# Performance work log

Measured on AMD Instinct MI355X. Metric: run time of the kernel, lower is better.

## Reference

```python
import jax, jax.numpy as jnp
import numpy as np

DIM = 768
HID = 24576          # hidden_features (SAE dictionary size)
DENSE = 3072         # dense_hidden_features (MLP width)
NUM_LAYERS = 12
L = NUM_LAYERS * 2   # forward requires x.shape[1] == num_layers*2 (broadcast with decoder_b2)
B = 64
K = 16               # num_active_features


def setup_inputs() -> dict:
    key = jax.random.key(0)
    ks = jax.random.split(key, 10)
    s1 = 1.0 / np.sqrt(DIM)
    s2 = 1.0 / np.sqrt(DENSE)
    s3 = 1.0 / np.sqrt(HID)
    return {
        "x": jax.random.normal(ks[0], (B, L, DIM), dtype=jnp.float32),
        "encoder_w1": jax.random.uniform(ks[1], (DENSE, DIM), jnp.float32, -s1, s1),
        "encoder_b1": jnp.zeros((DENSE,), jnp.float32),
        "encoder_w2": jax.random.uniform(ks[2], (HID, DENSE), jnp.float32, -s2, s2),
        "encoder_b2": jnp.zeros((HID,), jnp.float32),
        "decoder_w1": jax.random.uniform(ks[3], (DENSE, HID), jnp.float32, -s3, s3),
        "decoder_b1": jnp.zeros((DENSE,), jnp.float32),
        "decoder_w2": jax.random.uniform(ks[4], (DIM, DENSE), jnp.float32, -s2, s2),
        "decoder_b2": jax.random.uniform(ks[5], (1, L, DIM), jnp.float32, -s1, s1),
    }


def reference(x, encoder_w1, encoder_b1, encoder_w2, encoder_b2,
              decoder_w1, decoder_b1, decoder_w2, decoder_b2):
    # subtract per-(layer,dim) decoder bias, dense encode, GELU (exact, matches nn.GELU)
    h = jax.nn.gelu(jnp.einsum('blc,dc->bld', x - decoder_b2, encoder_w1) + encoder_b1,
                    approximate=False)                         # [B, L, DENSE]
    z = jnp.einsum('bld,nd->bln', h, encoder_w2) + encoder_b2  # [B, L, HID]
    # topk mask: keep only K largest per (b, l), zero the rest (scatter of ones)
    _, idx = jax.lax.top_k(z, K)                               # [B, L, K]
    b_idx = jnp.arange(z.shape[0])[:, None, None]
    l_idx = jnp.arange(z.shape[1])[None, :, None]
    mask = jnp.zeros_like(z).at[b_idx, l_idx, idx].set(1.0)
    z = jax.nn.relu(z * mask)                                  # act_fn = ReLU
    # dense decode (full GEMM over mostly-zero hidden dim, as in the original)
    d = jax.nn.gelu(jnp.einsum('bln,dn->bld', z, decoder_w1) + decoder_b1,
                    approximate=False)                         # [B, L, DENSE]
    return jnp.einsum('bld,cd->blc', d, decoder_w2) + decoder_b2  # [B, L, DIM]
```

## Files before the change

### kernel.cpp

```cpp
#include <hip/hip_runtime.h>
#include <hip/hip_fp16.h>

#define DIM 768
#define HID 24576
#define DENSE 3072
#define LL 24
#define MROWS 1536
#define KSEL 16
#define NC 24
#define CAP 40
#define MF_TOT 96
#define ENC2_NT 96
#define DELTA 2e-3f

typedef _Float16 f16;
typedef __attribute__((ext_vector_type(8))) _Float16 f16x8;
typedef __attribute__((ext_vector_type(4))) float f32x4;
typedef const __attribute__((address_space(1))) char* gcp;
typedef __attribute__((address_space(3))) char* lcp;

__device__ __forceinline__ float gelu_exact(float x) {
    return 0.5f * x * (1.0f + erff(x * 0.7071067811865476f));
}

__device__ __forceinline__ void split8(const float4& v0, const float4& v1,
                                       f16x8& hi, f16x8& lo) {
    float vv[8] = {v0.x, v0.y, v0.z, v0.w, v1.x, v1.y, v1.z, v1.w};
#pragma unroll
    for (int j = 0; j < 8; ++j) {
        f16 h = (f16)vv[j];
        hi[j] = h;
        lo[j] = (f16)((vv[j] - (float)h) * 2048.0f);
    }
}


template <int KTOT, int RFTOT>
__global__ __launch_bounds__(256) void apack_kernel(
    const float* __restrict__ src, f16* __restrict__ dst) {
    int c = blockIdx.x * 4 + (threadIdx.x >> 6);
    int lane = threadIdx.x & 63;
    int rf = c % RFTOT, ks = c / RFTOT;
    int m = rf * 16 + (lane & 15);
    int k = ks * 32 + (lane >> 4) * 8;
    const float4* s = (const float4*)(src + (size_t)m * (KTOT * 32) + k);
    f16x8 hi, lo;
    split8(s[0], s[1], hi, lo);
    char* base = (char*)dst + (size_t)c * 2048 + lane * 16;
    *(f16x8*)base = hi;
    *(f16x8*)(base + 1024) = lo;
}

__global__ __launch_bounds__(256) void prep1_kernel(
    const float* __restrict__ x, const float* __restrict__ b2,
    f16* __restrict__ xcpk,
    const float* __restrict__ w1src, f16* __restrict__ W1pk) {
    int lane = threadIdx.x & 63;
    if (blockIdx.x < 576) {
        int c = blockIdx.x * 4 + (threadIdx.x >> 6);
        int rf = c % MF_TOT, ks = c / MF_TOT;
        int m = rf * 16 + (lane & 15);
        int k = ks * 32 + (lane >> 4) * 8;
        const float4* sx = (const float4*)(x + (size_t)m * DIM + k);
        const float4* sb = (const float4*)(b2 + (m % LL) * DIM + k);
        float4 v0 = sx[0], v1 = sx[1], b0 = sb[0], b1 = sb[1];
        v0.x -= b0.x; v0.y -= b0.y; v0.z -= b0.z; v0.w -= b0.w;
        v1.x -= b1.x; v1.y -= b1.y; v1.z -= b1.z; v1.w -= b1.w;
        f16x8 hi, lo;
        split8(v0, v1, hi, lo);
        char* base = (char*)xcpk + (size_t)c * 2048 + lane * 16;
        *(f16x8*)base = hi;
        *(f16x8*)(base + 1024) = lo;
    } else {
        int c = (blockIdx.x - 576) * 4 + (threadIdx.x >> 6);
        int nf = c & 7; int t = c >> 3; int ks = t % 24; int nb = t / 24;
        int n = nb * 128 + nf * 16 + (lane & 15);
        int k = ks * 32 + (lane >> 4) * 8;
        const float4* s = (const float4*)(w1src + (size_t)n * DIM + k);
        f16x8 hi, lo;
        split8(s[0], s[1], hi, lo);
        char* base = (char*)W1pk + (size_t)c * 2048 + lane * 16;
        *(f16x8*)base = hi;
        *(f16x8*)(base + 1024) = lo;
    }
}

template <int KTOT>
__global__ __launch_bounds__(256) void wpack_kernel(
    const float* __restrict__ src, f16* __restrict__ dst, int row0) {
    int c = blockIdx.x * 4 + (threadIdx.x >> 6);
    int lane = threadIdx.x & 63;
    int nf = c & 7; int t = c >> 3; int ks = t % KTOT; int nb = t / KTOT;
    int n = row0 + nb * 128 + nf * 16 + (lane & 15);
    int k = ks * 32 + (lane >> 4) * 8;
    const float4* s = (const float4*)(src + (size_t)n * (KTOT * 32) + k);
    f16x8 hi, lo;
    split8(s[0], s[1], hi, lo);
    char* base = (char*)dst + (size_t)c * 2048 + lane * 16;
    *(f16x8*)base = hi;
    *(f16x8*)(base + 1024) = lo;
}

__global__ __launch_bounds__(256) void prep2_kernel(
    const float* __restrict__ h, f16* __restrict__ ApkHi,
    const float* __restrict__ w2, f16* __restrict__ Wpk) {
    int lane = threadIdx.x & 63;
    if (blockIdx.x < 2304) {
        int c = blockIdx.x * 4 + (threadIdx.x >> 6);
        int rf = c % MF_TOT, ks = c / MF_TOT;
        int m = rf * 16 + (lane & 15);
        int k = ks * 32 + (lane >> 4) * 8;
        const float4* s = (const float4*)(h + (size_t)m * DENSE + k);
        float4 v0 = s[0], v1 = s[1];
        float vv[8] = {v0.x, v0.y, v0.z, v0.w, v1.x, v1.y, v1.z, v1.w};
        f16x8 hi;
#pragma unroll
        for (int j = 0; j < 8; ++j) hi[j] = (f16)vv[j];
        *(f16x8*)((char*)ApkHi + (size_t)c * 1024 + lane * 16) = hi;
    } else {
        int c = (blockIdx.x - 2304) * 4 + (threadIdx.x >> 6);
        int nf = c & 7; int t = c >> 3; int ks = t % 96; int nb = t / 96;
        int n = nb * 128 + nf * 16 + (lane & 15);
        int k = ks * 32 + (lane >> 4) * 8;
        const float4* s = (const float4*)(w2 + (size_t)n * DENSE + k);
        float4 v0 = s[0], v1 = s[1];
        float vv[8] = {v0.x, v0.y, v0.z, v0.w, v1.x, v1.y, v1.z, v1.w};
        f16x8 hi;
#pragma unroll
        for (int j = 0; j < 8; ++j) hi[j] = (f16)vv[j];
        *(f16x8*)((char*)Wpk + (size_t)c * 1024 + lane * 16) = hi;
    }
}

__global__ __launch_bounds__(256) void transpose_w1_kernel(
    const float* __restrict__ src, __half* __restrict__ dst) {
    __shared__ float tile[32][33];
    const int c0 = blockIdx.x * 32;
    const int r0 = blockIdx.y * 32;
    const int tx = threadIdx.x & 31, ty = threadIdx.x >> 5;
#pragma unroll
    for (int i = 0; i < 32; i += 8)
        tile[ty + i][tx] = src[(size_t)(r0 + ty + i) * HID + c0 + tx];
    __syncthreads();
#pragma unroll
    for (int i = 0; i < 32; i += 8)
        dst[(size_t)(c0 + ty + i) * DENSE + r0 + tx] = __float2half(tile[tx][ty + i]);
}

template <int KTOT, int EPI>
__global__ __launch_bounds__(256, 2) void mfma_nt_kernel(
    const f16* __restrict__ Apk, const f16* __restrict__ Wpk,
    const float* __restrict__ bias, float* __restrict__ C,
    int N, int n0g) {
    __shared__ __align__(16) char lds[2][32768];
    const int tid = threadIdx.x;
    const int lane = tid & 63, wave = tid >> 6;
    const int mb = blockIdx.x, nb = blockIdx.y;
    const int wr = wave >> 1, wc = wave & 1;
    const char* ApkB = (const char*)Apk;
    const char* WpkB = (const char*)Wpk;

    f32x4 accH[4][4] = {}; f32x4 accL[4][4] = {};

    auto stage = [&](int buf, int ks) {
        const char* Ar = ApkB + (size_t)(ks * MF_TOT + mb * 8) * 2048;
        const char* Wr = WpkB + (size_t)(nb * KTOT + ks) * 16384;
#pragma unroll
        for (int q = 0; q < 8; ++q) {
            int c = wave * 8 + q;
            const char* src = (c < 16 ? Ar + c * 1024 : Wr + (c - 16) * 1024) + lane * 16;
            char* dst = &lds[buf][c * 1024];
            __builtin_amdgcn_global_load_lds((gcp)src, (lcp)dst, 16, 0, 0);
        }
    };

    stage(0, 0);
    for (int ks = 0; ks < KTOT; ++ks) {
        int cur = ks & 1;
        __syncthreads();
        if (ks + 1 < KTOT) stage(cur ^ 1, ks + 1);
        const char* Bf = lds[cur];
        f16x8 Ahi[4], Alo[4], Whi[4], Wlo[4];
#pragma unroll
        for (int i = 0; i < 4; ++i) {
            Ahi[i] = *(const f16x8*)(Bf + ((wr * 4 + i) * 2 + 0) * 1024 + lane * 16);
            Alo[i] = *(const f16x8*)(Bf + ((wr * 4 + i) * 2 + 1) * 1024 + lane * 16);
            Whi[i] = *(const f16x8*)(Bf + 16384 + ((wc * 4 + i) * 2 + 0) * 1024 + lane * 16);
            Wlo[i] = *(const f16x8*)(Bf + 16384 + ((wc * 4 + i) * 2 + 1) * 1024 + lane * 16);
        }
#pragma unroll
        for (int i = 0; i < 4; ++i)
#pragma unroll
            for (int j = 0; j < 4; ++j) {
                accH[i][j] = __builtin_amdgcn_mfma_f32_16x16x32_f16(Ahi[i], Whi[j], accH[i][j], 0, 0, 0);
                accL[i][j] = __builtin_amdgcn_mfma_f32_16x16x32_f16(Ahi[i], Wlo[j], accL[i][j], 0, 0, 0);
                accL[i][j] = __builtin_amdgcn_mfma_f32_16x16x32_f16(Alo[i], Whi[j], accL[i][j], 0, 0, 0);
            }
    }
    const int rbase = mb * 128 + wr * 64 + (lane >> 4) * 4;
    const int cb = n0g + nb * 128 + wc * 64 + (lane & 15);
#pragma unroll
    for (int j = 0; j < 4; ++j) {
        int col = cb + j * 16;
        float bn = (EPI == 2) ? 0.0f : bias[col];
#pragma unroll
        for (int i = 0; i < 4; ++i) {
#pragma unroll
            for (int e = 0; e < 4; ++e) {
                int row = rbase + i * 16 + e;
                float v = accH[i][j][e] + accL[i][j][e] * (1.0f / 2048.0f);
                if (EPI == 1)       v = gelu_exact(v + bn);
                else if (EPI == 0)  v += bn;
                else                v += bias[(row % LL) * N + col];
                C[(size_t)row * N + col] = v;
            }
        }
    }
}

__global__ __launch_bounds__(256, 4) void mfma64_kernel(
    const f16* __restrict__ Apk, const f16* __restrict__ Wpk,
    const float* __restrict__ bias, float* __restrict__ C) {
    __shared__ __align__(16) char lds[2][16384];
    const int tid = threadIdx.x;
    const int lane = tid & 63, wave = tid >> 6;
    const int mb = blockIdx.x, nbi = blockIdx.y;
    const int wr = wave >> 1, wc = wave & 1;
    const char* ApkB = (const char*)Apk;
    const char* WpkB = (const char*)Wpk;

    f32x4 accH[2][2] = {}; f32x4 accL[2][2] = {};

    auto stage = [&](int buf, int ks) {
        const char* Ar = ApkB + (size_t)(ks * 96 + mb * 4) * 2048;
        const char* Wr = WpkB + (((size_t)(nbi >> 1) * 96 + ks) * 8 + (nbi & 1) * 4) * 2048;
#pragma unroll
        for (int q = 0; q < 2; ++q) {
            __builtin_amdgcn_global_load_lds(
                (gcp)(Ar + tid * 16 + q * 4096),
                (lcp)(&lds[buf][0] + (tid & ~63) * 16 + q * 4096), 16, 0, 0);
            __builtin_amdgcn_global_load_lds(
                (gcp)(Wr + tid * 16 + q * 4096),
                (lcp)(&lds[buf][8192] + (tid & ~63) * 16 + q * 4096), 16, 0, 0);
        }
    };

    stage(0, 0);
    for (int ks = 0; ks < 96; ++ks) {
        int cur = ks & 1;
        __syncthreads();
        if (ks + 1 < 96) stage(cur ^ 1, ks + 1);
        const char* Bf = lds[cur];
        f16x8 Ahi[2], Alo[2], Whi[2], Wlo[2];
#pragma unroll
        for (int i = 0; i < 2; ++i) {
            Ahi[i] = *(const f16x8*)(Bf + (wr * 2 + i) * 2048 + lane * 16);
            Alo[i] = *(const f16x8*)(Bf + (wr * 2 + i) * 2048 + 1024 + lane * 16);
            Whi[i] = *(const f16x8*)(Bf + 8192 + (wc * 2 + i) * 2048 + lane * 16);
            Wlo[i] = *(const f16x8*)(Bf + 8192 + (wc * 2 + i) * 2048 + 1024 + lane * 16);
        }
#pragma unroll
        for (int i = 0; i < 2; ++i)
#pragma unroll
            for (int j = 0; j < 2; ++j) {
                accH[i][j] = __builtin_amdgcn_mfma_f32_16x16x32_f16(Ahi[i], Whi[j], accH[i][j], 0, 0, 0);
                accL[i][j] = __builtin_amdgcn_mfma_f32_16x16x32_f16(Ahi[i], Wlo[j], accL[i][j], 0, 0, 0);
                accL[i][j] = __builtin_amdgcn_mfma_f32_16x16x32_f16(Alo[i], Whi[j], accL[i][j], 0, 0, 0);
            }
    }
    const int rbase = mb * 64 + wr * 32 + (lane >> 4) * 4;
    const int cb = nbi * 64 + wc * 32 + (lane & 15);
#pragma unroll
    for (int j = 0; j < 2; ++j) {
        int col = cb + j * 16;
#pragma unroll
        for (int i = 0; i < 2; ++i) {
#pragma unroll
            for (int e = 0; e < 4; ++e) {
                int row = rbase + i * 16 + e;
                float v = accH[i][j][e] + accL[i][j][e] * (1.0f / 2048.0f)
                        + bias[(row % LL) * DIM + col];
                C[(size_t)row * DIM + col] = v;
            }
        }
    }
}

__global__ __launch_bounds__(512, 4) void enc2v3_kernel(
    const f16* __restrict__ Apk, const f16* __restrict__ Wpk,
    const float* __restrict__ b2, __half* __restrict__ z) {
    __shared__ __align__(16) char lds[3][24576];
    const int tid = threadIdx.x;
    const int lane = tid & 63, wave = tid >> 6;
    int f = blockIdx.y * 6 + blockIdx.x;
    int ff = (f & 7) * 144 + (f >> 3);
    const int mb = ff % 6, nb = ff / 6;
    const int wr = wave >> 1, wc = wave & 1;
    const char* ApkB = (const char*)Apk;
    const char* WpkB = (const char*)Wpk;
    f32x4 acc[4][4] = {};

    auto stage = [&](int t) {
        if (t >= ENC2_NT) return;
        char* dst = lds[t % 3];
        const char* Asrc = ApkB + ((size_t)t * MF_TOT + mb * 16) * 1024;
        __builtin_amdgcn_global_load_lds((gcp)(Asrc + tid * 16),
                                         (lcp)(dst + (tid & ~63) * 16), 16, 0, 0);
        __builtin_amdgcn_global_load_lds((gcp)(Asrc + tid * 16 + 8192),
                                         (lcp)(dst + (tid & ~63) * 16 + 8192), 16, 0, 0);
        const char* Wsrc = WpkB + ((size_t)nb * 96 + t) * 8192;
        __builtin_amdgcn_global_load_lds((gcp)(Wsrc + tid * 16),
                                         (lcp)(dst + 16384 + (tid & ~63) * 16), 16, 0, 0);
    };

    stage(0); stage(1);
    asm volatile("s_waitcnt vmcnt(3)" ::: "memory");
    __builtin_amdgcn_s_barrier();

    for (int t = 0; t < ENC2_NT; ++t) {
        const char* Bf = lds[t % 3];
        f16x8 Af[4], Wf[4];
#pragma unroll
        for (int i = 0; i < 4; ++i) {
            Af[i] = *(const f16x8*)(Bf + (wr * 4 + i) * 1024 + lane * 16);
            Wf[i] = *(const f16x8*)(Bf + 16384 + (wc * 4 + i) * 1024 + lane * 16);
        }
        stage(t + 2);
        __builtin_amdgcn_s_setprio(1);
#pragma unroll
        for (int i = 0; i < 4; ++i)
#pragma unroll
            for (int j = 0; j < 4; ++j)
                acc[i][j] = __builtin_amdgcn_mfma_f32_16x16x32_f16(Af[i], Wf[j], acc[i][j], 0, 0, 0);
        __builtin_amdgcn_s_setprio(0);
        if (t < ENC2_NT - 2)      asm volatile("s_waitcnt vmcnt(3)" ::: "memory");
        else if (t < ENC2_NT - 1) asm volatile("s_waitcnt vmcnt(0)" ::: "memory");
        if (t < ENC2_NT - 1) __builtin_amdgcn_s_barrier();
    }
    const int rbase = mb * 256 + wr * 64 + (lane >> 4) * 4;
    const int cb = nb * 128 + wc * 64 + (lane & 15);
#pragma unroll
    for (int j = 0; j < 4; ++j) {
        int col = cb + j * 16;
        float bn = b2[col];
#pragma unroll
        for (int r = 0; r < 4; ++r)
#pragma unroll
            for (int e = 0; e < 4; ++e)
                z[(size_t)(rbase + r * 16 + e) * HID + col] = __float2half(acc[r][j][e] + bn);
    }
}

__global__ __launch_bounds__(512) void topksel_kernel(
    const __half* __restrict__ z, int* __restrict__ candi, int* __restrict__ candn) {
    __shared__ unsigned short keys[HID];
    __shared__ unsigned hist[4][256];
    __shared__ int sB1, sA, sT, scnt;
    const int row = blockIdx.x, tid = threadIdx.x;
    const int lane = tid & 63, wave = tid >> 6;
    const int hrep = wave & 3;
    const uint4* zr = reinterpret_cast<const uint4*>(z + (size_t)row * HID);
    if (tid < 256) { hist[0][tid] = 0; hist[1][tid] = 0; hist[2][tid] = 0; hist[3][tid] = 0; }
    if (tid == 0) scnt = 0;
    __syncthreads();
#pragma unroll
    for (int i = 0; i < 6; ++i) {
        uint4 v = zr[tid + i * 512];
        unsigned w[4] = {v.x, v.y, v.z, v.w};
        int base = (tid + i * 512) * 8;
#pragma unroll
        for (int q = 0; q < 4; ++q)
#pragma unroll
            for (int s = 0; s < 2; ++s) {
                unsigned b = (w[q] >> (16 * s)) & 0xFFFFu;
                unsigned kk = b ^ ((b & 0x8000u) ? 0xFFFFu : 0x8000u);
                keys[base + q * 2 + s] = (unsigned short)kk;
                atomicAdd(&hist[hrep][kk >> 8], 1u);
            }
    }
    __syncthreads();
    if (wave == 0) {
        const int b0 = 252 - 4 * lane;
        int bc[4];
#pragma unroll
        for (int j = 0; j < 4; ++j)
            bc[j] = (int)(hist[0][b0 + j] + hist[1][b0 + j] + hist[2][b0 + j] + hist[3][b0 + j]);
        int part = bc[0] + bc[1] + bc[2] + bc[3];
        int incl = part;
#pragma unroll
        for (int off = 1; off < 64; off <<= 1) {
            int v = __shfl_up(incl, off);
            if (lane >= off) incl += v;
        }
        int pre = incl - part;
        if (pre < NC && NC <= incl) {
            int cum = pre;
            for (int j = 3; j >= 0; --j) {
                if (cum + bc[j] >= NC) { sB1 = b0 + j; sA = cum; break; }
                cum += bc[j];
            }
        }
    }
    __syncthreads();
    const int B1 = sB1, t2 = NC - sA;
    __syncthreads();
    if (tid < 256) { hist[0][tid] = 0; hist[1][tid] = 0; hist[2][tid] = 0; hist[3][tid] = 0; }
    __syncthreads();
#pragma unroll
    for (int i = 0; i < 48; ++i) {
        unsigned kk = keys[tid + i * 512];
        if ((int)(kk >> 8) == B1) atomicAdd(&hist[hrep][kk & 0xFF], 1u);
    }
    __syncthreads();
    if (wave == 0) {
        const int b0 = 252 - 4 * lane;
        int bc[4];
#pragma unroll
        for (int j = 0; j < 4; ++j)
            bc[j] = (int)(hist[0][b0 + j] + hist[1][b0 + j] + hist[2][b0 + j] + hist[3][b0 + j]);
        int part = bc[0] + bc[1] + bc[2] + bc[3];
        int incl = part;
#pragma unroll
        for (int off = 1; off < 64; off <<= 1) {
            int v = __shfl_up(incl, off);
            if (lane >= off) incl += v;
        }
        int pre = incl - part;
        if (pre < t2 && t2 <= incl) {
            int cum = pre;
            for (int j = 3; j >= 0; --j) {
                if (cum + bc[j] >= t2) { sT = (B1 << 8) | (b0 + j); break; }
                cum += bc[j];
            }
        }
    }
    __syncthreads();
    const unsigned T = (unsigned)sT;
#pragma unroll
    for (int i = 0; i < 48; ++i) {
        int idx = tid + i * 512;
        if ((unsigned)keys[idx] >= T) {
            int p = atomicAdd(&scnt, 1);
            if (p < CAP) candi[(size_t)row * CAP + p] = idx;
        }
    }
    __syncthreads();
    if (tid == 0) candn[row] = min(scnt, CAP);
}

__global__ __launch_bounds__(256) void resolve16_kernel(
    const __half* __restrict__ z, const float* __restrict__ h,
    const float* __restrict__ w2, const float* __restrict__ b2,
    const int* __restrict__ candi, const int* __restrict__ candn,
    float* __restrict__ tkv, int* __restrict__ tki) {
    const int row = blockIdx.x, tid = threadIdx.x;
    const int lane = tid & 63, wave = tid >> 6;
    __shared__ float hs[DENSE];
    __shared__ float av[64];
    __shared__ int ci[64];
    __shared__ int bnd[CAP];
    __shared__ int nb_s;
    const int cnt = candn[row];
    const float4* hr = reinterpret_cast<const float4*>(h + (size_t)row * DENSE);
#pragma unroll
    for (int j = 0; j < 3; ++j)
        reinterpret_cast<float4*>(hs)[tid + j * 256] = hr[tid + j * 256];
    if (wave == 0) {
        float myv = -1e30f;
        int myi = 0x7fffffff;
        if (lane < cnt) {
            myi = candi[(size_t)row * CAP + lane];
            myv = __half2float(z[(size_t)row * HID + myi]);
        }
        int rank = 0;
#pragma unroll
        for (int o = 0; o < CAP; ++o) {
            float ov = __shfl(myv, o);
            int oi = __shfl(myi, o);
            rank += ((ov > myv) || (ov == myv && oi < myi)) ? 1 : 0;
        }
        unsigned long long m15 = __ballot(rank == 15);
        int sl = (int)__builtin_ctzll(m15);
        float v16 = __shfl(myv, sl);
        bool band = (lane < cnt) && (fabsf(myv - v16) <= DELTA);
        unsigned long long bm = __ballot(band);
        if (lane == 0) nb_s = (int)__popcll(bm);
        if (band) {
            int p = (int)__popcll(bm & ((1ull << lane) - 1ull));
            bnd[p] = lane;
        }
        av[lane] = myv;
        ci[lane] = myi;
    }
    __syncthreads();
    const int nbn = nb_s;
    for (int b = wave; b < nbn; b += 4) {
        int c = bnd[b];
        int n = ci[c];
        const float4* wr = reinterpret_cast<const float4*>(w2 + (size_t)n * DENSE);
        float p = 0.0f;
#pragma unroll
        for (int j = 0; j < 12; ++j) {
            float4 a = reinterpret_cast<const float4*>(hs)[lane + j * 64];
            float4 w = wr[lane + j * 64];
            p += a.x * w.x + a.y * w.y + a.z * w.z + a.w * w.w;
        }
#pragma unroll
        for (int off = 32; off >= 1; off >>= 1) p += __shfl_down(p, off);
        if (lane == 0) av[c] = p + b2[n];
    }
    __syncthreads();
    if (wave == 0) {
        float v = av[lane];
        int idx = ci[lane];
        int rank = 0;
#pragma unroll
        for (int o = 0; o < CAP; ++o) {
            float ov = __shfl(v, o);
            int oi = __shfl(idx, o);
            rank += ((ov > v) || (ov == v && oi < idx)) ? 1 : 0;
        }
        if (lane < cnt && rank < KSEL) {
            tkv[row * KSEL + rank] = fmaxf(v, 0.0f);
            tki[row * KSEL + rank] = idx;
        }
    }
}

__global__ __launch_bounds__(256) void sparse_decode_kernel(
    const float* __restrict__ tkv, const int* __restrict__ tki,
    const __half* __restrict__ w1t, const float* __restrict__ b1,
    float* __restrict__ D) {
    const int row = blockIdx.x, tid = threadIdx.x;
    __shared__ float sv[KSEL];
    __shared__ int si[KSEL];
    if (tid < KSEL) { sv[tid] = tkv[row * KSEL + tid]; si[tid] = tki[row * KSEL + tid]; }
    __syncthreads();
    float acc[3][4] = {};
#pragma unroll 1
    for (int k = 0; k < KSEL; ++k) {
        const float v = sv[k];
        const uint2* wr = reinterpret_cast<const uint2*>(w1t + (size_t)si[k] * DENSE);
#pragma unroll
        for (int j = 0; j < 3; ++j) {
            uint2 u = wr[tid + j * 256];
            float2 f0 = __half22float2(*reinterpret_cast<const __half2*>(&u.x));
            float2 f1 = __half22float2(*reinterpret_cast<const __half2*>(&u.y));
            acc[j][0] = fmaf(v, f0.x, acc[j][0]);
            acc[j][1] = fmaf(v, f0.y, acc[j][1]);
            acc[j][2] = fmaf(v, f1.x, acc[j][2]);
            acc[j][3] = fmaf(v, f1.y, acc[j][3]);
        }
    }
#pragma unroll
    for (int j = 0; j < 3; ++j) {
        int dd = (tid + j * 256) * 4;
        float4 o;
        o.x = gelu_exact(acc[j][0] + b1[dd]);
        o.y = gelu_exact(acc[j][1] + b1[dd + 1]);
        o.z = gelu_exact(acc[j][2] + b1[dd + 2]);
        o.w = gelu_exact(acc[j][3] + b1[dd + 3]);
        *reinterpret_cast<float4*>(D + (size_t)row * DENSE + dd) = o;
    }
}

extern "C" void kernel_launch(void* const* d_in, const int* in_sizes, int n_in,
                              void* d_out, int out_size, void* d_ws, size_t ws_size,
                              hipStream_t stream) {
    const float* x      = (const float*)d_in[0];
    const float* enc_w1 = (const float*)d_in[1];
    const float* enc_b1 = (const float*)d_in[2];
    const float* enc_w2 = (const float*)d_in[3];
    const float* enc_b2 = (const float*)d_in[4];
    const float* dec_w1 = (const float*)d_in[5];
    const float* dec_b1 = (const float*)d_in[6];
    const float* dec_w2 = (const float*)d_in[7];
    const float* dec_b2 = (const float*)d_in[8];
    float* out = (float*)d_out;

    char* ws = (char*)d_ws;
    size_t off = 0;
    f16*    Wpk = (f16*)(ws + off);
    __half* w1t = (__half*)(ws + off); off += (size_t)HID * DENSE * 2;
    __half* z    = (__half*)(ws + off); off += (size_t)MROWS * HID * 2;
    f16*    ApkHi = (f16*)(ws + off);  off += (size_t)MROWS * DENSE * 2;
    f16*    Dpk  = (f16*)(ws + off);   off += (size_t)MROWS * DENSE * 4;
    float*  h    = (float*)(ws + off); off += (size_t)MROWS * DENSE * 4;
    float*  dbuf = (float*)(ws + off); off += (size_t)MROWS * DENSE * 4;
    f16*    W1pk = (f16*)(ws + off);
    f16*    Wd2pk = (f16*)(ws + off);  off += (size_t)DENSE * DIM * 4;
    f16*    xcpk = (f16*)(ws + off);   off += (size_t)MROWS * DIM * 4;
    float*  tkv  = (float*)(ws + off); off += (size_t)MROWS * KSEL * 4;
    int*    tki  = (int*)(ws + off);   off += (size_t)MROWS * KSEL * 4;
    int*    candi = (int*)(ws + off);  off += (size_t)MROWS * CAP * 4;
    int*    candn = (int*)(ws + off);  off += (size_t)MROWS * 4;

    prep1_kernel<<<576 + 1152, 256, 0, stream>>>(x, dec_b2, xcpk, enc_w1, W1pk);
    mfma_nt_kernel<24, 1><<<dim3(12, 24), 256, 0, stream>>>(
        xcpk, W1pk, enc_b1, h, DENSE, 0);
    prep2_kernel<<<2304 + 36864, 256, 0, stream>>>(h, ApkHi, enc_w2, Wpk);
    enc2v3_kernel<<<dim3(6, 192), 512, 0, stream>>>(ApkHi, Wpk, enc_b2, z);
    transpose_w1_kernel<<<dim3(HID / 32, DENSE / 32), 256, 0, stream>>>(dec_w1, w1t);
    topksel_kernel<<<MROWS, 512, 0, stream>>>(z, candi, candn);
    resolve16_kernel<<<MROWS, 256, 0, stream>>>(
        z, h, enc_w2, enc_b2, candi, candn, tkv, tki);
    sparse_decode_kernel<<<MROWS, 256, 0, stream>>>(tkv, tki, w1t, dec_b1, dbuf);
    apack_kernel<96, 96><<<96 * 96 / 4, 256, 0, stream>>>(dbuf, Dpk);
    wpack_kernel<96><<<6 * 96 * 8 / 4, 256, 0, stream>>>(dec_w2, Wd2pk, 0);
    mfma64_kernel<<<dim3(24, 12), 256, 0, stream>>>(Dpk, Wd2pk, dec_b2, out);
}
```

Baseline: 587.8 us.

## Replace decoder weight transpose with row-wise sparse decode in LDS

Removes the full transpose of decoder_w1 into a half-precision workspace and instead has one block per dense output row load that row of decoder_w1 into shared memory as fp16, then gather the 16 selected entries for every token. The output is written transposed and repacked into the MFMA hi/lo layout by a new pack kernel. The decoder_w2 packing is folded into prep2 to save a launch. This cuts a large transpose read/write pass but reads all of decoder_w1 once per call, uses 48KB LDS per block, and the repack now reads with strided gathers.

```diff
diff --git a/kernel.cpp b/kernel.cpp
--- a/kernel.cpp
+++ b/kernel.cpp
@@ -34,22 +34,6 @@
     }
 }
 
-
-template <int KTOT, int RFTOT>
-__global__ __launch_bounds__(256) void apack_kernel(
-    const float* __restrict__ src, f16* __restrict__ dst) {
-    int c = blockIdx.x * 4 + (threadIdx.x >> 6);
-    int lane = threadIdx.x & 63;
-    int rf = c % RFTOT, ks = c / RFTOT;
-    int m = rf * 16 + (lane & 15);
-    int k = ks * 32 + (lane >> 4) * 8;
-    const float4* s = (const float4*)(src + (size_t)m * (KTOT * 32) + k);
-    f16x8 hi, lo;
-    split8(s[0], s[1], hi, lo);
-    char* base = (char*)dst + (size_t)c * 2048 + lane * 16;
-    *(f16x8*)base = hi;
-    *(f16x8*)(base + 1024) = lo;
-}
 
 __global__ __launch_bounds__(256) void prep1_kernel(
     const float* __restrict__ x, const float* __restrict__ b2,
@@ -85,25 +69,10 @@
     }
 }
 
-template <int KTOT>
-__global__ __launch_bounds__(256) void wpack_kernel(
-    const float* __restrict__ src, f16* __restrict__ dst, int row0) {
-    int c = blockIdx.x * 4 + (threadIdx.x >> 6);
-    int lane = threadIdx.x & 63;
-    int nf = c & 7; int t = c >> 3; int ks = t % KTOT; int nb = t / KTOT;
-    int n = row0 + nb * 128 + nf * 16 + (lane & 15);
-    int k = ks * 32 + (lane >> 4) * 8;
-    const float4* s = (const float4*)(src + (size_t)n * (KTOT * 32) + k);
-    f16x8 hi, lo;
-    split8(s[0], s[1], hi, lo);
-    char* base = (char*)dst + (size_t)c * 2048 + lane * 16;
-    *(f16x8*)base = hi;
-    *(f16x8*)(base + 1024) = lo;
-}
-
 __global__ __launch_bounds__(256) void prep2_kernel(
     const float* __restrict__ h, f16* __restrict__ ApkHi,
-    const float* __restrict__ w2, f16* __restrict__ Wpk) {
+    const float* __restrict__ w2, f16* __restrict__ Wpk,
+    const float* __restrict__ wd2, f16* __restrict__ Wd2pk) {
     int lane = threadIdx.x & 63;
     if (blockIdx.x < 2304) {
         int c = blockIdx.x * 4 + (threadIdx.x >> 6);
@@ -117,7 +86,7 @@
 #pragma unroll
         for (int j = 0; j < 8; ++j) hi[j] = (f16)vv[j];
         *(f16x8*)((char*)ApkHi + (size_t)c * 1024 + lane * 16) = hi;
-    } else {
+    } else if (blockIdx.x < 39168) {
         int c = (blockIdx.x - 2304) * 4 + (threadIdx.x >> 6);
         int nf = c & 7; int t = c >> 3; int ks = t % 96; int nb = t / 96;
         int n = nb * 128 + nf * 16 + (lane & 15);
@@ -129,22 +98,18 @@
 #pragma unroll
         for (int j = 0; j < 8; ++j) hi[j] = (f16)vv[j];
         *(f16x8*)((char*)Wpk + (size_t)c * 1024 + lane * 16) = hi;
-    }
-}
-
-__global__ __launch_bounds__(256) void transpose_w1_kernel(
-    const float* __restrict__ src, __half* __restrict__ dst) {
-    __shared__ float tile[32][33];
-    const int c0 = blockIdx.x * 32;
-    const int r0 = blockIdx.y * 32;
-    const int tx = threadIdx.x & 31, ty = threadIdx.x >> 5;
-#pragma unroll
-    for (int i = 0; i < 32; i += 8)
-        tile[ty + i][tx] = src[(size_t)(r0 + ty + i) * HID + c0 + tx];
-    __syncthreads();
-#pragma unroll
-    for (int i = 0; i < 32; i += 8)
-        dst[(size_t)(c0 + ty + i) * DENSE + r0 + tx] = __float2half(tile[tx][ty + i]);
+    } else {
+        int c = (blockIdx.x - 39168) * 4 + (threadIdx.x >> 6);
+        int nf = c & 7; int t = c >> 3; int ks = t % 96; int nb = t / 96;
+        int n = nb * 128 + nf * 16 + (lane & 15);
+        int k = ks * 32 + (lane >> 4) * 8;
+        const float4* s = (const float4*)(wd2 + (size_t)n * DENSE + k);
+        f16x8 hi, lo;
+        split8(s[0], s[1], hi, lo);
+        char* base = (char*)Wd2pk + (size_t)c * 2048 + lane * 16;
+        *(f16x8*)base = hi;
+        *(f16x8*)(base + 1024) = lo;
+    }
 }
 
 template <int KTOT, int EPI>
@@ -527,41 +492,62 @@
     }
 }
 
-__global__ __launch_bounds__(256) void sparse_decode_kernel(
+__global__ __launch_bounds__(512) void sparse_decodeT_kernel(
     const float* __restrict__ tkv, const int* __restrict__ tki,
-    const __half* __restrict__ w1t, const float* __restrict__ b1,
-    float* __restrict__ D) {
-    const int row = blockIdx.x, tid = threadIdx.x;
-    __shared__ float sv[KSEL];
-    __shared__ int si[KSEL];
-    if (tid < KSEL) { sv[tid] = tkv[row * KSEL + tid]; si[tid] = tki[row * KSEL + tid]; }
-    __syncthreads();
-    float acc[3][4] = {};
-#pragma unroll 1
-    for (int k = 0; k < KSEL; ++k) {
-        const float v = sv[k];
-        const uint2* wr = reinterpret_cast<const uint2*>(w1t + (size_t)si[k] * DENSE);
-#pragma unroll
-        for (int j = 0; j < 3; ++j) {
-            uint2 u = wr[tid + j * 256];
-            float2 f0 = __half22float2(*reinterpret_cast<const __half2*>(&u.x));
-            float2 f1 = __half22float2(*reinterpret_cast<const __half2*>(&u.y));
-            acc[j][0] = fmaf(v, f0.x, acc[j][0]);
-            acc[j][1] = fmaf(v, f0.y, acc[j][1]);
-            acc[j][2] = fmaf(v, f1.x, acc[j][2]);
-            acc[j][3] = fmaf(v, f1.y, acc[j][3]);
-        }
-    }
-#pragma unroll
-    for (int j = 0; j < 3; ++j) {
-        int dd = (tid + j * 256) * 4;
-        float4 o;
-        o.x = gelu_exact(acc[j][0] + b1[dd]);
-        o.y = gelu_exact(acc[j][1] + b1[dd + 1]);
-        o.z = gelu_exact(acc[j][2] + b1[dd + 2]);
-        o.w = gelu_exact(acc[j][3] + b1[dd + 3]);
-        *reinterpret_cast<float4*>(D + (size_t)row * DENSE + dd) = o;
-    }
+    const float* __restrict__ w1, const float* __restrict__ b1,
+    float* __restrict__ dT) {
+    __shared__ __half wrow[HID];
+    const int r = blockIdx.x, tid = threadIdx.x;
+    const float4* wr4 = reinterpret_cast<const float4*>(w1 + (size_t)r * HID);
+#pragma unroll
+    for (int i = 0; i < 12; ++i) {
+        float4 v = wr4[tid + i * 512];
+        int p = (tid + i * 512) * 4;
+        uint2 packed;
+        __half2 h01 = __floats2half2_rn(v.x, v.y);
+        __half2 h23 = __floats2half2_rn(v.z, v.w);
+        packed.x = *reinterpret_cast<const unsigned*>(&h01);
+        packed.y = *reinterpret_cast<const unsigned*>(&h23);
+        *reinterpret_cast<uint2*>(&wrow[p]) = packed;
+    }
+    const float b1r = b1[r];
+    __syncthreads();
+#pragma unroll
+    for (int c = 0; c < 3; ++c) {
+        const int row = c * 512 + tid;
+        float sv[KSEL];
+        int si[KSEL];
+#pragma unroll
+        for (int k = 0; k < KSEL; ++k) {
+            sv[k] = tkv[row * KSEL + k];
+            si[k] = tki[row * KSEL + k];
+        }
+        float acc = 0.0f;
+#pragma unroll
+        for (int k = 0; k < KSEL; ++k)
+            acc = fmaf(sv[k], __half2float(wrow[si[k]]), acc);
+        dT[(size_t)r * MROWS + row] = gelu_exact(acc + b1r);
+    }
+}
+
+__global__ __launch_bounds__(256) void dpackT_kernel(
+    const float* __restrict__ dT, f16* __restrict__ dst) {
+    int c = blockIdx.x * 4 + (threadIdx.x >> 6);
+    int lane = threadIdx.x & 63;
+    int rf = c % 96, ks = c / 96;
+    int m = rf * 16 + (lane & 15);
+    int k0 = ks * 32 + (lane >> 4) * 8;
+    f16x8 hi, lo;
+#pragma unroll
+    for (int j = 0; j < 8; ++j) {
+        float v = dT[(size_t)(k0 + j) * MROWS + m];
+        f16 hh = (f16)v;
+        hi[j] = hh;
+        lo[j] = (f16)((v - (float)hh) * 2048.0f);
+    }
+    char* base = (char*)dst + (size_t)c * 2048 + lane * 16;
+    *(f16x8*)base = hi;
+    *(f16x8*)(base + 1024) = lo;
 }
 
 extern "C" void kernel_launch(void* const* d_in, const int* in_sizes, int n_in,
@@ -580,13 +566,12 @@
 
     char* ws = (char*)d_ws;
     size_t off = 0;
-    f16*    Wpk = (f16*)(ws + off);
-    __half* w1t = (__half*)(ws + off); off += (size_t)HID * DENSE * 2;
+    f16*    Wpk  = (f16*)(ws + off);   off += (size_t)HID * DENSE * 2;
     __half* z    = (__half*)(ws + off); off += (size_t)MROWS * HID * 2;
     f16*    ApkHi = (f16*)(ws + off);  off += (size_t)MROWS * DENSE * 2;
     f16*    Dpk  = (f16*)(ws + off);   off += (size_t)MROWS * DENSE * 4;
     float*  h    = (float*)(ws + off); off += (size_t)MROWS * DENSE * 4;
-    float*  dbuf = (float*)(ws + off); off += (size_t)MROWS * DENSE * 4;
+    float*  dT   = (float*)(ws + off); off += (size_t)DENSE * MROWS * 4;
     f16*    W1pk = (f16*)(ws + off);
     f16*    Wd2pk = (f16*)(ws + off);  off += (size_t)DENSE * DIM * 4;
     f16*    xcpk = (f16*)(ws + off);   off += (size_t)MROWS * DIM * 4;
@@ -598,14 +583,13 @@
     prep1_kernel<<<576 + 1152, 256, 0, stream>>>(x, dec_b2, xcpk, enc_w1, W1pk);
     mfma_nt_kernel<24, 1><<<dim3(12, 24), 256, 0, stream>>>(
         xcpk, W1pk, enc_b1, h, DENSE, 0);
-    prep2_kernel<<<2304 + 36864, 256, 0, stream>>>(h, ApkHi, enc_w2, Wpk);
+    prep2_kernel<<<2304 + 36864 + 1152, 256, 0, stream>>>(
+        h, ApkHi, enc_w2, Wpk, dec_w2, Wd2pk);
     enc2v3_kernel<<<dim3(6, 192), 512, 0, stream>>>(ApkHi, Wpk, enc_b2, z);
-    transpose_w1_kernel<<<dim3(HID / 32, DENSE / 32), 256, 0, stream>>>(dec_w1, w1t);
     topksel_kernel<<<MROWS, 512, 0, stream>>>(z, candi, candn);
     resolve16_kernel<<<MROWS, 256, 0, stream>>>(
         z, h, enc_w2, enc_b2, candi, candn, tkv, tki);
-    sparse_decode_kernel<<<MROWS, 256, 0, stream>>>(tkv, tki, w1t, dec_b1, dbuf);
-    apack_kernel<96, 96><<<96 * 96 / 4, 256, 0, stream>>>(dbuf, Dpk);
-    wpack_kernel<96><<<6 * 96 * 8 / 4, 256, 0, stream>>>(dec_w2, Wd2pk, 0);
+    sparse_decodeT_kernel<<<DENSE, 512, 0, stream>>>(tkv, tki, dec_w1, dec_b1, dT);
+    dpackT_kernel<<<96 * 96 / 4, 256, 0, stream>>>(dT, Dpk);
     mfma64_kernel<<<dim3(24, 12), 256, 0, stream>>>(Dpk, Wd2pk, dec_b2, out);
 }
```

Measured after the change: 541.9 us (median of 2 runs). 7.8% less time.
